# Performance work log

Hardware: AMD Instinct MI355X
Metric: run time of the kernel (lower is better)

The kernel has to match this reference:

```python
import jax, jax.numpy as jnp
import numpy as np

B, D_IN, H, V_TOT, T = 131072, 128, 256, 6, 6  # total_vocab = vocab_size+1 = 6


def setup_inputs() -> dict:
    key = jax.random.key(0)
    ks = jax.random.split(key, 16)
    s = 0.02
    return {
        "x": jax.random.normal(ks[0], (B, D_IN), jnp.float32),
        "W_enc": jax.random.normal(ks[1], (D_IN, H), jnp.float32) * s,
        "b_enc": jnp.zeros((H,), jnp.float32),
        "W_embed": jax.random.normal(ks[2], (V_TOT, H), jnp.float32) * s,
        "b_embed": jnp.zeros((H,), jnp.float32),
        "W_z": jax.random.normal(ks[3], (2 * H, H), jnp.float32) * s,
        "b_z": jnp.zeros((H,), jnp.float32),
        "W_r": jax.random.normal(ks[4], (2 * H, H), jnp.float32) * s,
        "b_r": jnp.zeros((H,), jnp.float32),
        "W_h": jax.random.normal(ks[5], (2 * H, H), jnp.float32) * s,
        "b_h": jnp.zeros((H,), jnp.float32),
        "W_out": jax.random.normal(ks[6], (H, V_TOT), jnp.float32) * s,
        "b_out": jnp.zeros((V_TOT,), jnp.float32),
        "start_embed": jax.random.normal(ks[7], (H,), jnp.float32) * 0.01,
    }


def reference(x, W_enc, b_enc, W_embed, b_embed, W_z, b_z, W_r, b_r, W_h, b_h,
              W_out, b_out, start_embed):
    h0 = x @ W_enc + b_enc                      # encoder: (B, H)
    bsz = h0.shape[0]
    keys = jax.random.split(jax.random.key(42), T)

    def gru(xin, h):
        c = jnp.concatenate([xin, h], axis=-1)
        z = jax.nn.sigmoid(c @ W_z + b_z)
        r = jax.nn.sigmoid(c @ W_r + b_r)
        cr = jnp.concatenate([xin, r * h], axis=-1)
        h_t = jnp.tanh(cr @ W_h + b_h)
        return (1 - z) * h + z * h_t

    def step(carry, key_t):
        h, prev_embed, total_lp, stopped, lengths = carry
        h = gru(prev_embed, h)
        logits = h @ W_out + b_out              # (B, V_TOT)
        token = jax.random.categorical(key_t, logits)  # training=True sampling
        logp = jax.nn.log_softmax(logits)
        active = (~stopped).astype(logits.dtype)
        lp = jnp.take_along_axis(logp, token[:, None], axis=1)[:, 0] * active
        total_lp = total_lp + lp
        onehot = jax.nn.one_hot(token, V_TOT, dtype=logits.dtype) * active[:, None]
        is_stop = token == (V_TOT - 1)
        lengths = lengths + ((~stopped) & (~is_stop)).astype(jnp.int32)
        stopped = stopped | is_stop
        prev_embed = jax.lax.stop_gradient(onehot) @ W_embed + b_embed
        return (h, prev_embed, total_lp, stopped, lengths), onehot

    init = (h0,
            jnp.broadcast_to(start_embed, (bsz, H)),
            jnp.zeros((bsz,), h0.dtype),
            jnp.zeros((bsz,), bool),
            jnp.zeros((bsz,), jnp.int32))
    (h, _, total_log_prob, _, lengths), onehots = jax.lax.scan(step, init, keys)
    # onehots: (T, B, V_TOT) -> message (B, T*V_TOT)
    message = jnp.transpose(onehots, (1, 0, 2)).reshape(bsz, T * V_TOT)
    return message, total_log_prob, lengths
```

## Files before the change

kernel.cpp:

```cpp
#include <hip/hip_runtime.h>
#include <stdint.h>

#define NB   131072
#define DIN  128
#define HD   256
#define VT   6
#define TS   6
#define BM   32
#define NTH  256

typedef __attribute__((ext_vector_type(8))) short bfrag;
typedef __attribute__((ext_vector_type(4))) short bh4;
typedef __attribute__((ext_vector_type(4))) float f32x4;

struct Keys { uint32_t a[6]; uint32_t b[6]; };

#define HPS(p, kc, nt, ln2, j) ((((p) * 8 + (kc)) * 1040) + (nt) * 512 + (ln2) * 8 + (j))

__host__ __device__ inline void tf2x32(uint32_t k0, uint32_t k1,
                                       uint32_t c0, uint32_t c1,
                                       uint32_t& o0, uint32_t& o1) {
  uint32_t ks2 = k0 ^ k1 ^ 0x1BD11BDAu;
  uint32_t x0 = c0 + k0, x1 = c1 + k1;
#define TFR(d) { x0 += x1; x1 = (x1 << (d)) | (x1 >> (32 - (d))); x1 ^= x0; }
  TFR(13) TFR(15) TFR(26) TFR(6)
  x0 += k1;  x1 += ks2 + 1u;
  TFR(17) TFR(29) TFR(16) TFR(24)
  x0 += ks2; x1 += k0 + 2u;
  TFR(13) TFR(15) TFR(26) TFR(6)
  x0 += k0;  x1 += k1 + 3u;
  TFR(17) TFR(29) TFR(16) TFR(24)
  x0 += k1;  x1 += ks2 + 4u;
  TFR(13) TFR(15) TFR(26) TFR(6)
  x0 += ks2; x1 += k0 + 5u;
#undef TFR
  o0 = x0; o1 = x1;
}

__device__ __forceinline__ unsigned short f2bf(float x) {
  uint32_t b = __float_as_uint(x);
  uint32_t r = b + 0x7FFFu + ((b >> 16) & 1u);
  return (unsigned short)(r >> 16);
}
__device__ __forceinline__ float bf2f(unsigned short u) {
  return __uint_as_float(((uint32_t)u) << 16);
}
__device__ __forceinline__ float sigf(float v) { return 1.0f / (1.0f + expf(-v)); }

#define MFMA16(a, b, c) __builtin_amdgcn_mfma_f32_16x16x32_bf16((a), (b), (c), 0, 0, 0)

__device__ __forceinline__ f32x4 prod6(const bfrag A[3], bfrag B0, bfrag B1, bfrag B2,
                                       f32x4 c) {
  c = MFMA16(A[0], B0, c);
  c = MFMA16(A[0], B1, c);
  c = MFMA16(A[1], B0, c);
  c = MFMA16(A[1], B1, c);
  c = MFMA16(A[0], B2, c);
  c = MFMA16(A[2], B0, c);
  return c;
}

__global__ void pre_kernel(const float* __restrict__ W_enc,
                           const float* __restrict__ W_embed,
                           const float* __restrict__ b_embed,
                           const float* __restrict__ start_embed,
                           const float* __restrict__ W_z, const float* __restrict__ b_z,
                           const float* __restrict__ W_r, const float* __restrict__ b_r,
                           const float* __restrict__ W_h, const float* __restrict__ b_h,
                           float* __restrict__ pre,
                           unsigned short* __restrict__ encf,
                           unsigned short* __restrict__ zf,
                           unsigned short* __restrict__ rf,
                           unsigned short* __restrict__ hf) {
  const int bid = blockIdx.x;
  if (bid < 24) {
    __shared__ float xin[HD];
    const int c = bid & 7, g = bid >> 3, j = threadIdx.x;
    float v;
    if (c < 6)       v = W_embed[c * HD + j] + b_embed[j];
    else if (c == 6) v = b_embed[j];
    else             v = start_embed[j];
    xin[j] = v;
    __syncthreads();
    const float* Wg = (g == 0) ? W_z : (g == 1) ? W_r : W_h;
    const float* bg = (g == 0) ? b_z : (g == 1) ? b_r : b_h;
    float acc = bg[j];
    for (int k = 0; k < HD; ++k) acc += xin[k] * Wg[k * HD + j];
    pre[(g * 8 + c) * HD + j] = acc;
    return;
  }
  int id = (bid - 24) * 256 + threadIdx.x;
  const float* src; unsigned short* dst; int kc, mt, lane, KC, krow0;
  if (id < 4096) {
    lane = id & 63; mt = (id >> 6) & 15; kc = id >> 10;
    src = W_enc; dst = encf; KC = 4; krow0 = 0;
  } else {
    int rem = id - 4096; int g = rem >> 13; int rr = rem & 8191;
    lane = rr & 63; mt = (rr >> 6) & 15; kc = rr >> 10;
    src = (g == 0) ? W_z : (g == 1) ? W_r : W_h;
    dst = (g == 0) ? zf  : (g == 1) ? rf  : hf;
    KC = 8; krow0 = 256;
  }
  const int m  = mt * 16 + (lane & 15);
  const int k0 = kc * 32 + ((lane >> 4) & 3) * 8;
  __align__(16) unsigned short P[3][8];
#pragma unroll
  for (int j = 0; j < 8; ++j) {
    float w = src[(size_t)(krow0 + k0 + j) * HD + m];
    unsigned short h1 = f2bf(w);  float r1 = w - bf2f(h1);
    unsigned short h2 = f2bf(r1); float r2 = r1 - bf2f(h2);
    P[0][j] = h1; P[1][j] = h2; P[2][j] = f2bf(r2);
  }
  for (int p = 0; p < 3; ++p) {
    unsigned short* d = dst + ((size_t)(p * KC + kc) * 16 + mt) * 512 + (size_t)lane * 8;
    *(uint4*)d = *(const uint4*)P[p];
  }
}

template<int KC, int NG>
__device__ __forceinline__ void gemm_pass(const unsigned short* __restrict__ f0,
                                          const unsigned short* __restrict__ f1,
                                          const unsigned short* hp_s,
                                          int wave, int lane,
                                          f32x4 acc0[4][2], f32x4 acc1[4][2]) {
#pragma unroll 1
  for (int kc = 0; kc < KC; ++kc) {
    bfrag B[3][2];
#pragma unroll
    for (int p = 0; p < 3; ++p)
#pragma unroll
      for (int nt = 0; nt < 2; ++nt)
        B[p][nt] = *(const bfrag*)&hp_s[HPS(p, kc, nt, lane, 0)];
#pragma unroll
    for (int mtl = 0; mtl < 4; ++mtl) {
      const int fo = (kc * 16 + wave * 4 + mtl) * 512 + lane * 8;
      bfrag A0[3], A1[3];
#pragma unroll
      for (int p = 0; p < 3; ++p) A0[p] = *(const bfrag*)(f0 + fo + p * (KC * 8192));
      if (NG == 2) {
#pragma unroll
        for (int p = 0; p < 3; ++p) A1[p] = *(const bfrag*)(f1 + fo + p * (KC * 8192));
      }
#pragma unroll
      for (int nt = 0; nt < 2; ++nt) {
        acc0[mtl][nt] = prod6(A0, B[0][nt], B[1][nt], B[2][nt], acc0[mtl][nt]);
        if (NG == 2)
          acc1[mtl][nt] = prod6(A1, B[0][nt], B[1][nt], B[2][nt], acc1[mtl][nt]);
      }
    }
  }
}

__launch_bounds__(NTH, 2)
__global__ void main_kernel(const float* __restrict__ x,
                            const float* __restrict__ b_enc,
                            const float* __restrict__ W_out,
                            const float* __restrict__ b_out,
                            const float* __restrict__ pre,
                            const unsigned short* __restrict__ encf,
                            const unsigned short* __restrict__ zf,
                            const unsigned short* __restrict__ rf,
                            const unsigned short* __restrict__ hf,
                            float* __restrict__ out, Keys keys) {
  __shared__ __align__(16) unsigned short hp_s[3 * 8 * 1040];
  __shared__ __align__(16) float wout2[VT * 8 * 40];
  __shared__ unsigned state[BM];
  __shared__ float tlp[BM];

  const int tid = threadIdx.x;
  const int wave = tid >> 6, lane = tid & 63;
  const int ln = lane & 15, qk = lane >> 4;
  const int b0 = blockIdx.x * BM;

  for (int i = tid; i < VT * HD; i += NTH) {
    int k = i & 255, v = i >> 8;
    wout2[(v * 8 + (k >> 5)) * 40 + (k & 31)] = W_out[k * VT + v];
  }
  if (tid < BM) { state[tid] = 7u; tlp[tid] = 0.f; }

  for (int i = tid; i < BM * DIN; i += NTH) {
    int row = i >> 7, k = i & 127;
    float v = x[(size_t)(b0 + row) * DIN + k];
    unsigned short h1 = f2bf(v);  float r1 = v - bf2f(h1);
    unsigned short h2 = f2bf(r1); float r2 = r1 - bf2f(h2);
    int kc = k >> 5, nt = row >> 4, lp = (row & 15) + 16 * ((k >> 3) & 3), j = k & 7;
    hp_s[HPS(0, kc, nt, lp, j)] = h1;
    hp_s[HPS(1, kc, nt, lp, j)] = h2;
    hp_s[HPS(2, kc, nt, lp, j)] = f2bf(r2);
  }
  __syncthreads();

  f32x4 acc0[4][2], acc1[4][2], z_s[4][2], hold[4][2];

#pragma unroll
  for (int mtl = 0; mtl < 4; ++mtl) {
    int mb = wave * 64 + mtl * 16 + qk * 4;
    f32x4 be = *(const f32x4*)&b_enc[mb];
#pragma unroll
    for (int nt = 0; nt < 2; ++nt) acc0[mtl][nt] = be;
  }
  gemm_pass<4, 1>(encf, nullptr, hp_s, wave, lane, acc0, acc1);
  __syncthreads();
#pragma unroll
  for (int mtl = 0; mtl < 4; ++mtl) {
    int mb = wave * 64 + mtl * 16 + qk * 4;
    int kc = mb >> 5, hi2 = (mb >> 3) & 3, j0 = mb & 7;
#pragma unroll
    for (int nt = 0; nt < 2; ++nt) {
      int lp = ln + 16 * hi2;
      bh4 P0, P1, P2;
#pragma unroll
      for (int j = 0; j < 4; ++j) {
        float v = acc0[mtl][nt][j];
        unsigned short h1 = f2bf(v);  float r1 = v - bf2f(h1);
        unsigned short h2 = f2bf(r1); float r2 = r1 - bf2f(h2);
        P0[j] = (short)h1; P1[j] = (short)h2; P2[j] = (short)f2bf(r2);
      }
      *(bh4*)&hp_s[HPS(0, kc, nt, lp, j0)] = P0;
      *(bh4*)&hp_s[HPS(1, kc, nt, lp, j0)] = P1;
      *(bh4*)&hp_s[HPS(2, kc, nt, lp, j0)] = P2;
    }
  }
  __syncthreads();

#pragma unroll 1
  for (int t = 0; t < TS; ++t) {
#pragma unroll
    for (int mtl = 0; mtl < 4; ++mtl) {
      int mb = wave * 64 + mtl * 16 + qk * 4;
#pragma unroll
      for (int nt = 0; nt < 2; ++nt) {
        int code = (int)(state[nt * 16 + ln] & 7u);
        acc0[mtl][nt] = *(const f32x4*)&pre[(0 * 8 + code) * 256 + mb];
        acc1[mtl][nt] = *(const f32x4*)&pre[(1 * 8 + code) * 256 + mb];
      }
    }
    gemm_pass<8, 2>(zf, rf, hp_s, wave, lane, acc0, acc1);
    __syncthreads();
#pragma unroll
    for (int mtl = 0; mtl < 4; ++mtl) {
      int mb = wave * 64 + mtl * 16 + qk * 4;
      int kc = mb >> 5, hi2 = (mb >> 3) & 3, j0 = mb & 7;
#pragma unroll
      for (int nt = 0; nt < 2; ++nt) {
        int lp = ln + 16 * hi2;
        bh4 H0 = *(const bh4*)&hp_s[HPS(0, kc, nt, lp, j0)];
        bh4 H1 = *(const bh4*)&hp_s[HPS(1, kc, nt, lp, j0)];
        bh4 H2 = *(const bh4*)&hp_s[HPS(2, kc, nt, lp, j0)];
        f32x4 ho, zv;
        bh4 P0, P1, P2;
#pragma unroll
        for (int j = 0; j < 4; ++j) {
          float hv = bf2f((unsigned short)H0[j]) + bf2f((unsigned short)H1[j])
                   + bf2f((unsigned short)H2[j]);
          ho[j] = hv;
          zv[j] = sigf(acc0[mtl][nt][j]);
          float rhv = sigf(acc1[mtl][nt][j]) * hv;
          unsigned short h1 = f2bf(rhv); float r1 = rhv - bf2f(h1);
          unsigned short h2 = f2bf(r1);  float r2 = r1 - bf2f(h2);
          P0[j] = (short)h1; P1[j] = (short)h2; P2[j] = (short)f2bf(r2);
        }
        z_s[mtl][nt] = zv; hold[mtl][nt] = ho;
        *(bh4*)&hp_s[HPS(0, kc, nt, lp, j0)] = P0;
        *(bh4*)&hp_s[HPS(1, kc, nt, lp, j0)] = P1;
        *(bh4*)&hp_s[HPS(2, kc, nt, lp, j0)] = P2;
      }
    }
    __syncthreads();

#pragma unroll
    for (int mtl = 0; mtl < 4; ++mtl) {
      int mb = wave * 64 + mtl * 16 + qk * 4;
#pragma unroll
      for (int nt = 0; nt < 2; ++nt) {
        int code = (int)(state[nt * 16 + ln] & 7u);
        acc0[mtl][nt] = *(const f32x4*)&pre[(2 * 8 + code) * 256 + mb];
      }
    }
    gemm_pass<8, 1>(hf, nullptr, hp_s, wave, lane, acc0, acc1);
    __syncthreads();
#pragma unroll
    for (int mtl = 0; mtl < 4; ++mtl) {
      int mb = wave * 64 + mtl * 16 + qk * 4;
      int kc = mb >> 5, hi2 = (mb >> 3) & 3, j0 = mb & 7;
#pragma unroll
      for (int nt = 0; nt < 2; ++nt) {
        int lp = ln + 16 * hi2;
        f32x4 z = z_s[mtl][nt], ho = hold[mtl][nt];
        bh4 P0, P1, P2;
#pragma unroll
        for (int j = 0; j < 4; ++j) {
          float ht = tanhf(acc0[mtl][nt][j]);
          float hn = (1.0f - z[j]) * ho[j] + z[j] * ht;
          unsigned short h1 = f2bf(hn); float r1 = hn - bf2f(h1);
          unsigned short h2 = f2bf(r1); float r2 = r1 - bf2f(h2);
          P0[j] = (short)h1; P1[j] = (short)h2; P2[j] = (short)f2bf(r2);
        }
        *(bh4*)&hp_s[HPS(0, kc, nt, lp, j0)] = P0;
        *(bh4*)&hp_s[HPS(1, kc, nt, lp, j0)] = P1;
        *(bh4*)&hp_s[HPS(2, kc, nt, lp, j0)] = P2;
      }
    }
    __syncthreads();

    {
      const int m = tid >> 3, q = tid & 7;
      float l[VT] = {0.f, 0.f, 0.f, 0.f, 0.f, 0.f};
#pragma unroll
      for (int c8 = 0; c8 < 4; ++c8) {
        bfrag H0 = *(const bfrag*)&hp_s[HPS(0, q, m >> 4, (m & 15) + 16 * c8, 0)];
        bfrag H1 = *(const bfrag*)&hp_s[HPS(1, q, m >> 4, (m & 15) + 16 * c8, 0)];
        bfrag H2 = *(const bfrag*)&hp_s[HPS(2, q, m >> 4, (m & 15) + 16 * c8, 0)];
        float hv[8];
#pragma unroll
        for (int j = 0; j < 8; ++j)
          hv[j] = bf2f((unsigned short)H0[j]) + bf2f((unsigned short)H1[j])
                + bf2f((unsigned short)H2[j]);
#pragma unroll
        for (int v = 0; v < VT; ++v) {
          f32x4 w0 = *(const f32x4*)&wout2[(v * 8 + q) * 40 + c8 * 8];
          f32x4 w1 = *(const f32x4*)&wout2[(v * 8 + q) * 40 + c8 * 8 + 4];
          l[v] += hv[0] * w0[0] + hv[1] * w0[1] + hv[2] * w0[2] + hv[3] * w0[3]
                + hv[4] * w1[0] + hv[5] * w1[1] + hv[6] * w1[2] + hv[7] * w1[3];
        }
      }
#pragma unroll
      for (int v = 0; v < VT; ++v) {
        l[v] += __shfl_xor(l[v], 1, 64);
        l[v] += __shfl_xor(l[v], 2, 64);
        l[v] += __shfl_xor(l[v], 4, 64);
      }
      if (q == 0) {
        const int row = b0 + m;
        unsigned st = state[m];
        if (!(st & 8u)) {
#pragma unroll
          for (int v = 0; v < VT; ++v) l[v] += b_out[v];
          const uint32_t k0 = keys.a[t], k1 = keys.b[t];
          float best = 0.f; int tok = 0;
#pragma unroll
          for (int v = 0; v < VT; ++v) {
            uint32_t j = (uint32_t)row * 6u + (uint32_t)v;
            uint32_t o0, o1;
            tf2x32(k0, k1, 0u, j, o0, o1);
            uint32_t bits = o0 ^ o1;
            float f = __uint_as_float((bits >> 9) | 0x3f800000u) - 1.0f;
            float u = (f > 0.f) ? f : 1.175494350822288e-38f;
            float lg1 = (float)log((double)u);
            float lg2 = (float)log((double)(-lg1));
            float val = l[v] + (-lg2);
            if (v == 0 || val > best) { best = val; tok = v; }
          }
          float lmax = l[0];
#pragma unroll
          for (int v = 1; v < VT; ++v) lmax = fmaxf(lmax, l[v]);
          float s = 0.f;
#pragma unroll
          for (int v = 0; v < VT; ++v) s += expf(l[v] - lmax);
          float lp = (l[tok] - lmax) - logf(s);
          tlp[m] += lp;
          const bool is_stop = (tok == VT - 1);
          unsigned len = ((st >> 4) & 7u) + (is_stop ? 0u : 1u);
#pragma unroll
          for (int v = 0; v < VT; ++v)
            out[(size_t)row * (TS * VT) + t * VT + v] = (v == tok) ? 1.0f : 0.0f;
          state[m] = (unsigned)tok | (is_stop ? 8u : 0u) | (len << 4);
        } else {
#pragma unroll
          for (int v = 0; v < VT; ++v)
            out[(size_t)row * (TS * VT) + t * VT + v] = 0.0f;
          state[m] = 6u | 8u | (st & 0x70u);
        }
      }
    }
    __syncthreads();
  }

  if (tid < BM) {
    const int row = b0 + tid;
    out[(size_t)NB * (TS * VT) + row]      = tlp[tid];
    out[(size_t)NB * (TS * VT) + NB + row] = (float)((state[tid] >> 4) & 7u);
  }
}

extern "C" void kernel_launch(void* const* d_in, const int* in_sizes, int n_in,
                              void* d_out, int out_size, void* d_ws, size_t ws_size,
                              hipStream_t stream) {
  (void)in_sizes; (void)n_in; (void)out_size; (void)ws_size;
  const float* x          = (const float*)d_in[0];
  const float* W_enc      = (const float*)d_in[1];
  const float* b_enc      = (const float*)d_in[2];
  const float* W_embed    = (const float*)d_in[3];
  const float* b_embed    = (const float*)d_in[4];
  const float* W_z        = (const float*)d_in[5];
  const float* b_z        = (const float*)d_in[6];
  const float* W_r        = (const float*)d_in[7];
  const float* b_r        = (const float*)d_in[8];
  const float* W_h        = (const float*)d_in[9];
  const float* b_h        = (const float*)d_in[10];
  const float* W_out      = (const float*)d_in[11];
  const float* b_out      = (const float*)d_in[12];
  const float* start_embed= (const float*)d_in[13];
  float* out = (float*)d_out;

  float* pre = (float*)d_ws;
  unsigned short* encf = (unsigned short*)((char*)d_ws + 24576);
  unsigned short* zfb  = (unsigned short*)((char*)d_ws + 221184);
  unsigned short* rfb  = (unsigned short*)((char*)d_ws + 614400);
  unsigned short* hfb  = (unsigned short*)((char*)d_ws + 1007616);

  pre_kernel<<<136, 256, 0, stream>>>(W_enc, W_embed, b_embed, start_embed,
                                      W_z, b_z, W_r, b_r, W_h, b_h,
                                      pre, encf, zfb, rfb, hfb);

  Keys K;
  for (int t = 0; t < 6; ++t) {
    uint32_t o0, o1;
    tf2x32(0u, 42u, 0u, (uint32_t)t, o0, o1);
    K.a[t] = o0; K.b[t] = o1;
  }

  main_kernel<<<NB / BM, NTH, 0, stream>>>(x, b_enc, W_out, b_out,
                                           pre, encf, zfb, rfb, hfb, out, K);
}
```

Before: 2.088 ms.

## Double batch tile to 64 rows, keep h in registers, parallelize sampling across lanes

```diff
diff --git a/kernel.cpp b/kernel.cpp
--- a/kernel.cpp
+++ b/kernel.cpp
@@ -6,8 +6,8 @@
 #define HD   256
 #define VT   6
 #define TS   6
-#define BM   32
-#define NTH  256
+#define BM   64
+#define NTH  512
 
 typedef __attribute__((ext_vector_type(8))) short bfrag;
 typedef __attribute__((ext_vector_type(4))) short bh4;
@@ -15,7 +15,7 @@
 
 struct Keys { uint32_t a[6]; uint32_t b[6]; };
 
-#define HPS(p, kc, nt, ln2, j) ((((p) * 8 + (kc)) * 1040) + (nt) * 512 + (ln2) * 8 + (j))
+#define HPS(p, kc, nt, lp, j) ((((p) * 8 + (kc)) * 2064) + (nt) * 512 + (lp) * 8 + (j))
 
 __host__ __device__ inline void tf2x32(uint32_t k0, uint32_t k1,
                                        uint32_t c0, uint32_t c1,
@@ -122,18 +122,18 @@
                                           const unsigned short* __restrict__ f1,
                                           const unsigned short* hp_s,
                                           int wave, int lane,
-                                          f32x4 acc0[4][2], f32x4 acc1[4][2]) {
+                                          f32x4 acc0[2][4], f32x4 acc1[2][4]) {
 #pragma unroll 1
   for (int kc = 0; kc < KC; ++kc) {
-    bfrag B[3][2];
+    bfrag B[3][4];
 #pragma unroll
     for (int p = 0; p < 3; ++p)
 #pragma unroll
-      for (int nt = 0; nt < 2; ++nt)
+      for (int nt = 0; nt < 4; ++nt)
         B[p][nt] = *(const bfrag*)&hp_s[HPS(p, kc, nt, lane, 0)];
 #pragma unroll
-    for (int mtl = 0; mtl < 4; ++mtl) {
-      const int fo = (kc * 16 + wave * 4 + mtl) * 512 + lane * 8;
+    for (int mtl = 0; mtl < 2; ++mtl) {
+      const int fo = (kc * 16 + wave * 2 + mtl) * 512 + lane * 8;
       bfrag A0[3], A1[3];
 #pragma unroll
       for (int p = 0; p < 3; ++p) A0[p] = *(const bfrag*)(f0 + fo + p * (KC * 8192));
@@ -142,7 +142,7 @@
         for (int p = 0; p < 3; ++p) A1[p] = *(const bfrag*)(f1 + fo + p * (KC * 8192));
       }
 #pragma unroll
-      for (int nt = 0; nt < 2; ++nt) {
+      for (int nt = 0; nt < 4; ++nt) {
         acc0[mtl][nt] = prod6(A0, B[0][nt], B[1][nt], B[2][nt], acc0[mtl][nt]);
         if (NG == 2)
           acc1[mtl][nt] = prod6(A1, B[0][nt], B[1][nt], B[2][nt], acc1[mtl][nt]);
@@ -162,8 +162,9 @@
                             const unsigned short* __restrict__ rf,
                             const unsigned short* __restrict__ hf,
                             float* __restrict__ out, Keys keys) {
-  __shared__ __align__(16) unsigned short hp_s[3 * 8 * 1040];
+  __shared__ __align__(16) unsigned short hp_s[3 * 8 * 2064];
   __shared__ __align__(16) float wout2[VT * 8 * 40];
+  __shared__ float boutL[8];
   __shared__ unsigned state[BM];
   __shared__ float tlp[BM];
 
@@ -176,6 +177,7 @@
     int k = i & 255, v = i >> 8;
     wout2[(v * 8 + (k >> 5)) * 40 + (k & 31)] = W_out[k * VT + v];
   }
+  if (tid < 8) boutL[tid] = (tid < VT) ? b_out[tid] : 0.f;
   if (tid < BM) { state[tid] = 7u; tlp[tid] = 0.f; }
 
   for (int i = tid; i < BM * DIN; i += NTH) {
@@ -190,28 +192,29 @@
   }
   __syncthreads();
 
-  f32x4 acc0[4][2], acc1[4][2], z_s[4][2], hold[4][2];
-
-#pragma unroll
-  for (int mtl = 0; mtl < 4; ++mtl) {
-    int mb = wave * 64 + mtl * 16 + qk * 4;
+  f32x4 acc0[2][4], acc1[2][4], z_s[2][4], hold[2][4];
+
+#pragma unroll
+  for (int mtl = 0; mtl < 2; ++mtl) {
+    int mb = (wave * 2 + mtl) * 16 + qk * 4;
     f32x4 be = *(const f32x4*)&b_enc[mb];
 #pragma unroll
-    for (int nt = 0; nt < 2; ++nt) acc0[mtl][nt] = be;
+    for (int nt = 0; nt < 4; ++nt) acc0[mtl][nt] = be;
   }
   gemm_pass<4, 1>(encf, nullptr, hp_s, wave, lane, acc0, acc1);
   __syncthreads();
 #pragma unroll
-  for (int mtl = 0; mtl < 4; ++mtl) {
-    int mb = wave * 64 + mtl * 16 + qk * 4;
-    int kc = mb >> 5, hi2 = (mb >> 3) & 3, j0 = mb & 7;
-#pragma unroll
-    for (int nt = 0; nt < 2; ++nt) {
-      int lp = ln + 16 * hi2;
+  for (int mtl = 0; mtl < 2; ++mtl) {
+    int mb = (wave * 2 + mtl) * 16 + qk * 4;
+    int kc = mb >> 5, hi2 = (mb >> 3) & 3, j0 = mb & 7, lp = ln + 16 * hi2;
+#pragma unroll
+    for (int nt = 0; nt < 4; ++nt) {
+      f32x4 o = acc0[mtl][nt];
+      hold[mtl][nt] = o;
       bh4 P0, P1, P2;
 #pragma unroll
       for (int j = 0; j < 4; ++j) {
-        float v = acc0[mtl][nt][j];
+        float v = o[j];
         unsigned short h1 = f2bf(v);  float r1 = v - bf2f(h1);
         unsigned short h2 = f2bf(r1); float r2 = r1 - bf2f(h2);
         P0[j] = (short)h1; P1[j] = (short)h2; P2[j] = (short)f2bf(r2);
@@ -226,10 +229,10 @@
 #pragma unroll 1
   for (int t = 0; t < TS; ++t) {
 #pragma unroll
-    for (int mtl = 0; mtl < 4; ++mtl) {
-      int mb = wave * 64 + mtl * 16 + qk * 4;
-#pragma unroll
-      for (int nt = 0; nt < 2; ++nt) {
+    for (int mtl = 0; mtl < 2; ++mtl) {
+      int mb = (wave * 2 + mtl) * 16 + qk * 4;
+#pragma unroll
+      for (int nt = 0; nt < 4; ++nt) {
         int code = (int)(state[nt * 16 + ln] & 7u);
         acc0[mtl][nt] = *(const f32x4*)&pre[(0 * 8 + code) * 256 + mb];
         acc1[mtl][nt] = *(const f32x4*)&pre[(1 * 8 + code) * 256 + mb];
@@ -238,29 +241,23 @@
     gemm_pass<8, 2>(zf, rf, hp_s, wave, lane, acc0, acc1);
     __syncthreads();
 #pragma unroll
-    for (int mtl = 0; mtl < 4; ++mtl) {
-      int mb = wave * 64 + mtl * 16 + qk * 4;
-      int kc = mb >> 5, hi2 = (mb >> 3) & 3, j0 = mb & 7;
-#pragma unroll
-      for (int nt = 0; nt < 2; ++nt) {
-        int lp = ln + 16 * hi2;
-        bh4 H0 = *(const bh4*)&hp_s[HPS(0, kc, nt, lp, j0)];
-        bh4 H1 = *(const bh4*)&hp_s[HPS(1, kc, nt, lp, j0)];
-        bh4 H2 = *(const bh4*)&hp_s[HPS(2, kc, nt, lp, j0)];
-        f32x4 ho, zv;
+    for (int mtl = 0; mtl < 2; ++mtl) {
+      int mb = (wave * 2 + mtl) * 16 + qk * 4;
+      int kc = mb >> 5, hi2 = (mb >> 3) & 3, j0 = mb & 7, lp = ln + 16 * hi2;
+#pragma unroll
+      for (int nt = 0; nt < 4; ++nt) {
+        f32x4 ho = hold[mtl][nt];
+        f32x4 zv;
         bh4 P0, P1, P2;
 #pragma unroll
         for (int j = 0; j < 4; ++j) {
-          float hv = bf2f((unsigned short)H0[j]) + bf2f((unsigned short)H1[j])
-                   + bf2f((unsigned short)H2[j]);
-          ho[j] = hv;
           zv[j] = sigf(acc0[mtl][nt][j]);
-          float rhv = sigf(acc1[mtl][nt][j]) * hv;
+          float rhv = sigf(acc1[mtl][nt][j]) * ho[j];
           unsigned short h1 = f2bf(rhv); float r1 = rhv - bf2f(h1);
           unsigned short h2 = f2bf(r1);  float r2 = r1 - bf2f(h2);
           P0[j] = (short)h1; P1[j] = (short)h2; P2[j] = (short)f2bf(r2);
         }
-        z_s[mtl][nt] = zv; hold[mtl][nt] = ho;
+        z_s[mtl][nt] = zv;
         *(bh4*)&hp_s[HPS(0, kc, nt, lp, j0)] = P0;
         *(bh4*)&hp_s[HPS(1, kc, nt, lp, j0)] = P1;
         *(bh4*)&hp_s[HPS(2, kc, nt, lp, j0)] = P2;
@@ -269,10 +266,10 @@
     __syncthreads();
 
 #pragma unroll
-    for (int mtl = 0; mtl < 4; ++mtl) {
-      int mb = wave * 64 + mtl * 16 + qk * 4;
-#pragma unroll
-      for (int nt = 0; nt < 2; ++nt) {
+    for (int mtl = 0; mtl < 2; ++mtl) {
+      int mb = (wave * 2 + mtl) * 16 + qk * 4;
+#pragma unroll
+      for (int nt = 0; nt < 4; ++nt) {
         int code = (int)(state[nt * 16 + ln] & 7u);
         acc0[mtl][nt] = *(const f32x4*)&pre[(2 * 8 + code) * 256 + mb];
       }
@@ -280,22 +277,22 @@
     gemm_pass<8, 1>(hf, nullptr, hp_s, wave, lane, acc0, acc1);
     __syncthreads();
 #pragma unroll
-    for (int mtl = 0; mtl < 4; ++mtl) {
-      int mb = wave * 64 + mtl * 16 + qk * 4;
-      int kc = mb >> 5, hi2 = (mb >> 3) & 3, j0 = mb & 7;
-#pragma unroll
-      for (int nt = 0; nt < 2; ++nt) {
-        int lp = ln + 16 * hi2;
-        f32x4 z = z_s[mtl][nt], ho = hold[mtl][nt];
+    for (int mtl = 0; mtl < 2; ++mtl) {
+      int mb = (wave * 2 + mtl) * 16 + qk * 4;
+      int kc = mb >> 5, hi2 = (mb >> 3) & 3, j0 = mb & 7, lp = ln + 16 * hi2;
+#pragma unroll
+      for (int nt = 0; nt < 4; ++nt) {
+        f32x4 z = z_s[mtl][nt], ho = hold[mtl][nt], hn;
         bh4 P0, P1, P2;
 #pragma unroll
         for (int j = 0; j < 4; ++j) {
           float ht = tanhf(acc0[mtl][nt][j]);
-          float hn = (1.0f - z[j]) * ho[j] + z[j] * ht;
-          unsigned short h1 = f2bf(hn); float r1 = hn - bf2f(h1);
-          unsigned short h2 = f2bf(r1); float r2 = r1 - bf2f(h2);
+          hn[j] = (1.0f - z[j]) * ho[j] + z[j] * ht;
+          unsigned short h1 = f2bf(hn[j]); float r1 = hn[j] - bf2f(h1);
+          unsigned short h2 = f2bf(r1);    float r2 = r1 - bf2f(h2);
           P0[j] = (short)h1; P1[j] = (short)h2; P2[j] = (short)f2bf(r2);
         }
+        hold[mtl][nt] = hn;
         *(bh4*)&hp_s[HPS(0, kc, nt, lp, j0)] = P0;
         *(bh4*)&hp_s[HPS(1, kc, nt, lp, j0)] = P1;
         *(bh4*)&hp_s[HPS(2, kc, nt, lp, j0)] = P2;
@@ -330,27 +327,33 @@
         l[v] += __shfl_xor(l[v], 2, 64);
         l[v] += __shfl_xor(l[v], 4, 64);
       }
+      const int row = b0 + m;
+      const int vq = (q < VT) ? q : 0;
+      float lq = l[vq] + boutL[vq];
+      {
+        uint32_t j = (uint32_t)row * 6u + (uint32_t)vq;
+        uint32_t o0, o1;
+        tf2x32(keys.a[t], keys.b[t], 0u, j, o0, o1);
+        uint32_t bits = o0 ^ o1;
+        float f = __uint_as_float((bits >> 9) | 0x3f800000u) - 1.0f;
+        float u = (f > 0.f) ? f : 1.175494350822288e-38f;
+        float lg1 = (float)log((double)u);
+        float lg2 = (float)log((double)(-lg1));
+        lq = lq + (-lg2);
+      }
+      float vv[VT];
+      const int lbase = lane & ~7;
+#pragma unroll
+      for (int v = 0; v < VT; ++v) vv[v] = __shfl(lq, lbase + v, 64);
       if (q == 0) {
-        const int row = b0 + m;
         unsigned st = state[m];
         if (!(st & 8u)) {
 #pragma unroll
-          for (int v = 0; v < VT; ++v) l[v] += b_out[v];
-          const uint32_t k0 = keys.a[t], k1 = keys.b[t];
+          for (int v = 0; v < VT; ++v) l[v] += boutL[v];
           float best = 0.f; int tok = 0;
 #pragma unroll
-          for (int v = 0; v < VT; ++v) {
-            uint32_t j = (uint32_t)row * 6u + (uint32_t)v;
-            uint32_t o0, o1;
-            tf2x32(k0, k1, 0u, j, o0, o1);
-            uint32_t bits = o0 ^ o1;
-            float f = __uint_as_float((bits >> 9) | 0x3f800000u) - 1.0f;
-            float u = (f > 0.f) ? f : 1.175494350822288e-38f;
-            float lg1 = (float)log((double)u);
-            float lg2 = (float)log((double)(-lg1));
-            float val = l[v] + (-lg2);
-            if (v == 0 || val > best) { best = val; tok = v; }
-          }
+          for (int v = 0; v < VT; ++v)
+            if (v == 0 || vv[v] > best) { best = vv[v]; tok = v; }
           float lmax = l[0];
 #pragma unroll
           for (int v = 1; v < VT; ++v) lmax = fmaxf(lmax, l[v]);
```

Result: faster. 2.033 ms (-2.6%).

## Compute output logits with MFMA, overlap Gumbel noise generation, keep h in registers

Applied to the files above, without the earlier changes.

```diff
diff --git a/kernel.cpp b/kernel.cpp
--- a/kernel.cpp
+++ b/kernel.cpp
@@ -15,7 +15,7 @@
 
 struct Keys { uint32_t a[6]; uint32_t b[6]; };
 
-#define HPS(p, kc, nt, ln2, j) ((((p) * 8 + (kc)) * 1040) + (nt) * 512 + (ln2) * 8 + (j))
+#define HPS(p, kc, nt, lp, j) ((((p) * 8 + (kc)) * 1040) + (nt) * 512 + (lp) * 8 + (j))
 
 __host__ __device__ inline void tf2x32(uint32_t k0, uint32_t k1,
                                        uint32_t c0, uint32_t c1,
@@ -67,11 +67,13 @@
                            const float* __restrict__ W_z, const float* __restrict__ b_z,
                            const float* __restrict__ W_r, const float* __restrict__ b_r,
                            const float* __restrict__ W_h, const float* __restrict__ b_h,
+                           const float* __restrict__ W_out,
                            float* __restrict__ pre,
                            unsigned short* __restrict__ encf,
                            unsigned short* __restrict__ zf,
                            unsigned short* __restrict__ rf,
-                           unsigned short* __restrict__ hf) {
+                           unsigned short* __restrict__ hf,
+                           unsigned short* __restrict__ woutf) {
   const int bid = blockIdx.x;
   if (bid < 24) {
     __shared__ float xin[HD];
@@ -87,6 +89,24 @@
     float acc = bg[j];
     for (int k = 0; k < HD; ++k) acc += xin[k] * Wg[k * HD + j];
     pre[(g * 8 + c) * HD + j] = acc;
+    return;
+  }
+  if (bid >= 136) {
+    int id2 = (bid - 136) * 256 + threadIdx.x;
+    int kc = id2 >> 6, lane = id2 & 63;
+    int m = lane & 15, k0 = kc * 32 + ((lane >> 4) & 3) * 8;
+    __align__(16) unsigned short P[3][8];
+#pragma unroll
+    for (int j = 0; j < 8; ++j) {
+      float w = (m < VT) ? W_out[(size_t)(k0 + j) * VT + m] : 0.f;
+      unsigned short h1 = f2bf(w);  float r1 = w - bf2f(h1);
+      unsigned short h2 = f2bf(r1); float r2 = r1 - bf2f(h2);
+      P[0][j] = h1; P[1][j] = h2; P[2][j] = f2bf(r2);
+    }
+    for (int p = 0; p < 3; ++p) {
+      unsigned short* d = woutf + ((size_t)(p * 8 + kc) * 512) + (size_t)lane * 8;
+      *(uint4*)d = *(const uint4*)P[p];
+    }
     return;
   }
   int id = (bid - 24) * 256 + threadIdx.x;
@@ -151,19 +171,40 @@
   }
 }
 
+__device__ __forceinline__ void gen_gumbel(float* __restrict__ gmb, int s, int b0,
+                                           int tile, int lane,
+                                           uint32_t ka, uint32_t kb) {
+  uint32_t basej = (uint32_t)(b0 + tile * 16) * 6u;
+#pragma unroll
+  for (int rep = 0; rep < 2; ++rep) {
+    int d = rep * 64 + lane;
+    if (d < 96) {
+      uint32_t o0, o1;
+      tf2x32(ka, kb, 0u, basej + (uint32_t)d, o0, o1);
+      uint32_t bits = o0 ^ o1;
+      float f = __uint_as_float((bits >> 9) | 0x3f800000u) - 1.0f;
+      float u = (f > 0.f) ? f : 1.175494350822288e-38f;
+      float lg1 = (float)log((double)u);
+      float lg2 = (float)log((double)(-lg1));
+      gmb[((s & 1) * 32 + tile * 16 + d / 6) * 6 + (d % 6)] = -lg2;
+    }
+  }
+}
+
 __launch_bounds__(NTH, 2)
 __global__ void main_kernel(const float* __restrict__ x,
                             const float* __restrict__ b_enc,
-                            const float* __restrict__ W_out,
                             const float* __restrict__ b_out,
                             const float* __restrict__ pre,
                             const unsigned short* __restrict__ encf,
                             const unsigned short* __restrict__ zf,
                             const unsigned short* __restrict__ rf,
                             const unsigned short* __restrict__ hf,
+                            const unsigned short* __restrict__ woutf,
                             float* __restrict__ out, Keys keys) {
   __shared__ __align__(16) unsigned short hp_s[3 * 8 * 1040];
-  __shared__ __align__(16) float wout2[VT * 8 * 40];
+  __shared__ float gmb_s[2 * 32 * 6];
+  __shared__ float boutL[16];
   __shared__ unsigned state[BM];
   __shared__ float tlp[BM];
 
@@ -172,10 +213,7 @@
   const int ln = lane & 15, qk = lane >> 4;
   const int b0 = blockIdx.x * BM;
 
-  for (int i = tid; i < VT * HD; i += NTH) {
-    int k = i & 255, v = i >> 8;
-    wout2[(v * 8 + (k >> 5)) * 40 + (k & 31)] = W_out[k * VT + v];
-  }
+  if (tid < 16) boutL[tid] = (tid < VT) ? b_out[tid] : 0.f;
   if (tid < BM) { state[tid] = 7u; tlp[tid] = 0.f; }
 
   for (int i = tid; i < BM * DIN; i += NTH) {
@@ -188,13 +226,14 @@
     hp_s[HPS(1, kc, nt, lp, j)] = h2;
     hp_s[HPS(2, kc, nt, lp, j)] = f2bf(r2);
   }
+  if (wave >= 2) gen_gumbel(gmb_s, 0, b0, wave - 2, lane, keys.a[0], keys.b[0]);
   __syncthreads();
 
   f32x4 acc0[4][2], acc1[4][2], z_s[4][2], hold[4][2];
 
 #pragma unroll
   for (int mtl = 0; mtl < 4; ++mtl) {
-    int mb = wave * 64 + mtl * 16 + qk * 4;
+    int mb = (wave * 4 + mtl) * 16 + qk * 4;
     f32x4 be = *(const f32x4*)&b_enc[mb];
 #pragma unroll
     for (int nt = 0; nt < 2; ++nt) acc0[mtl][nt] = be;
@@ -203,15 +242,16 @@
   __syncthreads();
 #pragma unroll
   for (int mtl = 0; mtl < 4; ++mtl) {
-    int mb = wave * 64 + mtl * 16 + qk * 4;
-    int kc = mb >> 5, hi2 = (mb >> 3) & 3, j0 = mb & 7;
+    int mb = (wave * 4 + mtl) * 16 + qk * 4;
+    int kc = mb >> 5, hi2 = (mb >> 3) & 3, j0 = mb & 7, lp = ln + 16 * hi2;
 #pragma unroll
     for (int nt = 0; nt < 2; ++nt) {
-      int lp = ln + 16 * hi2;
+      f32x4 o = acc0[mtl][nt];
+      hold[mtl][nt] = o;
       bh4 P0, P1, P2;
 #pragma unroll
       for (int j = 0; j < 4; ++j) {
-        float v = acc0[mtl][nt][j];
+        float v = o[j];
         unsigned short h1 = f2bf(v);  float r1 = v - bf2f(h1);
         unsigned short h2 = f2bf(r1); float r2 = r1 - bf2f(h2);
         P0[j] = (short)h1; P1[j] = (short)h2; P2[j] = (short)f2bf(r2);
@@ -227,7 +267,7 @@
   for (int t = 0; t < TS; ++t) {
 #pragma unroll
     for (int mtl = 0; mtl < 4; ++mtl) {
-      int mb = wave * 64 + mtl * 16 + qk * 4;
+      int mb = (wave * 4 + mtl) * 16 + qk * 4;
 #pragma unroll
       for (int nt = 0; nt < 2; ++nt) {
         int code = (int)(state[nt * 16 + ln] & 7u);
@@ -239,28 +279,22 @@
     __syncthreads();
 #pragma unroll
     for (int mtl = 0; mtl < 4; ++mtl) {
-      int mb = wave * 64 + mtl * 16 + qk * 4;
-      int kc = mb >> 5, hi2 = (mb >> 3) & 3, j0 = mb & 7;
+      int mb = (wave * 4 + mtl) * 16 + qk * 4;
+      int kc = mb >> 5, hi2 = (mb >> 3) & 3, j0 = mb & 7, lp = ln + 16 * hi2;
 #pragma unroll
       for (int nt = 0; nt < 2; ++nt) {
-        int lp = ln + 16 * hi2;
-        bh4 H0 = *(const bh4*)&hp_s[HPS(0, kc, nt, lp, j0)];
-        bh4 H1 = *(const bh4*)&hp_s[HPS(1, kc, nt, lp, j0)];
-        bh4 H2 = *(const bh4*)&hp_s[HPS(2, kc, nt, lp, j0)];
-        f32x4 ho, zv;
+        f32x4 ho = hold[mtl][nt];
+        f32x4 zv;
         bh4 P0, P1, P2;
 #pragma unroll
         for (int j = 0; j < 4; ++j) {
-          float hv = bf2f((unsigned short)H0[j]) + bf2f((unsigned short)H1[j])
-                   + bf2f((unsigned short)H2[j]);
-          ho[j] = hv;
           zv[j] = sigf(acc0[mtl][nt][j]);
-          float rhv = sigf(acc1[mtl][nt][j]) * hv;
+          float rhv = sigf(acc1[mtl][nt][j]) * ho[j];
           unsigned short h1 = f2bf(rhv); float r1 = rhv - bf2f(h1);
           unsigned short h2 = f2bf(r1);  float r2 = r1 - bf2f(h2);
           P0[j] = (short)h1; P1[j] = (short)h2; P2[j] = (short)f2bf(r2);
         }
-        z_s[mtl][nt] = zv; hold[mtl][nt] = ho;
+        z_s[mtl][nt] = zv;
         *(bh4*)&hp_s[HPS(0, kc, nt, lp, j0)] = P0;
         *(bh4*)&hp_s[HPS(1, kc, nt, lp, j0)] = P1;
         *(bh4*)&hp_s[HPS(2, kc, nt, lp, j0)] = P2;
@@ -270,7 +304,7 @@
 
 #pragma unroll
     for (int mtl = 0; mtl < 4; ++mtl) {
-      int mb = wave * 64 + mtl * 16 + qk * 4;
+      int mb = (wave * 4 + mtl) * 16 + qk * 4;
 #pragma unroll
       for (int nt = 0; nt < 2; ++nt) {
         int code = (int)(state[nt * 16 + ln] & 7u);
@@ -281,21 +315,21 @@
     __syncthreads();
 #pragma unroll
     for (int mtl = 0; mtl < 4; ++mtl) {
-      int mb = wave * 64 + mtl * 16 + qk * 4;
-      int kc = mb >> 5, hi2 = (mb >> 3) & 3, j0 = mb & 7;
+      int mb = (wave * 4 + mtl) * 16 + qk * 4;
+      int kc = mb >> 5, hi2 = (mb >> 3) & 3, j0 = mb & 7, lp = ln + 16 * hi2;
 #pragma unroll
       for (int nt = 0; nt < 2; ++nt) {
-        int lp = ln + 16 * hi2;
-        f32x4 z = z_s[mtl][nt], ho = hold[mtl][nt];
+        f32x4 z = z_s[mtl][nt], ho = hold[mtl][nt], hn;
         bh4 P0, P1, P2;
 #pragma unroll
         for (int j = 0; j < 4; ++j) {
           float ht = tanhf(acc0[mtl][nt][j]);
-          float hn = (1.0f - z[j]) * ho[j] + z[j] * ht;
-          unsigned short h1 = f2bf(hn); float r1 = hn - bf2f(h1);
-          unsigned short h2 = f2bf(r1); float r2 = r1 - bf2f(h2);
+          hn[j] = (1.0f - z[j]) * ho[j] + z[j] * ht;
+          unsigned short h1 = f2bf(hn[j]); float r1 = hn[j] - bf2f(h1);
+          unsigned short h2 = f2bf(r1);    float r2 = r1 - bf2f(h2);
           P0[j] = (short)h1; P1[j] = (short)h2; P2[j] = (short)f2bf(r2);
         }
+        hold[mtl][nt] = hn;
         *(bh4*)&hp_s[HPS(0, kc, nt, lp, j0)] = P0;
         *(bh4*)&hp_s[HPS(1, kc, nt, lp, j0)] = P1;
         *(bh4*)&hp_s[HPS(2, kc, nt, lp, j0)] = P2;
@@ -303,52 +337,33 @@
     }
     __syncthreads();
 
-    {
-      const int m = tid >> 3, q = tid & 7;
-      float l[VT] = {0.f, 0.f, 0.f, 0.f, 0.f, 0.f};
-#pragma unroll
-      for (int c8 = 0; c8 < 4; ++c8) {
-        bfrag H0 = *(const bfrag*)&hp_s[HPS(0, q, m >> 4, (m & 15) + 16 * c8, 0)];
-        bfrag H1 = *(const bfrag*)&hp_s[HPS(1, q, m >> 4, (m & 15) + 16 * c8, 0)];
-        bfrag H2 = *(const bfrag*)&hp_s[HPS(2, q, m >> 4, (m & 15) + 16 * c8, 0)];
-        float hv[8];
-#pragma unroll
-        for (int j = 0; j < 8; ++j)
-          hv[j] = bf2f((unsigned short)H0[j]) + bf2f((unsigned short)H1[j])
-                + bf2f((unsigned short)H2[j]);
-#pragma unroll
-        for (int v = 0; v < VT; ++v) {
-          f32x4 w0 = *(const f32x4*)&wout2[(v * 8 + q) * 40 + c8 * 8];
-          f32x4 w1 = *(const f32x4*)&wout2[(v * 8 + q) * 40 + c8 * 8 + 4];
-          l[v] += hv[0] * w0[0] + hv[1] * w0[1] + hv[2] * w0[2] + hv[3] * w0[3]
-                + hv[4] * w1[0] + hv[5] * w1[1] + hv[6] * w1[2] + hv[7] * w1[3];
-        }
-      }
-#pragma unroll
-      for (int v = 0; v < VT; ++v) {
-        l[v] += __shfl_xor(l[v], 1, 64);
-        l[v] += __shfl_xor(l[v], 2, 64);
-        l[v] += __shfl_xor(l[v], 4, 64);
-      }
-      if (q == 0) {
+    if (wave < 2) {
+      f32x4 lacc;
+#pragma unroll
+      for (int j = 0; j < 4; ++j) lacc[j] = boutL[qk * 4 + j];
+#pragma unroll 1
+      for (int kc = 0; kc < 8; ++kc) {
+        bfrag B0 = *(const bfrag*)&hp_s[HPS(0, kc, wave, lane, 0)];
+        bfrag B1 = *(const bfrag*)&hp_s[HPS(1, kc, wave, lane, 0)];
+        bfrag B2 = *(const bfrag*)&hp_s[HPS(2, kc, wave, lane, 0)];
+        bfrag A[3];
+#pragma unroll
+        for (int p = 0; p < 3; ++p)
+          A[p] = *(const bfrag*)(woutf + (p * 8 + kc) * 512 + lane * 8);
+        lacc = prod6(A, B0, B1, B2, lacc);
+      }
+      float l4 = __shfl(lacc[0], ln + 16, 64);
+      float l5 = __shfl(lacc[1], ln + 16, 64);
+      if (qk == 0) {
+        const int m = wave * 16 + ln;
         const int row = b0 + m;
         unsigned st = state[m];
         if (!(st & 8u)) {
-#pragma unroll
-          for (int v = 0; v < VT; ++v) l[v] += b_out[v];
-          const uint32_t k0 = keys.a[t], k1 = keys.b[t];
+          float l[VT] = {lacc[0], lacc[1], lacc[2], lacc[3], l4, l5};
           float best = 0.f; int tok = 0;
 #pragma unroll
           for (int v = 0; v < VT; ++v) {
-            uint32_t j = (uint32_t)row * 6u + (uint32_t)v;
-            uint32_t o0, o1;
-            tf2x32(k0, k1, 0u, j, o0, o1);
-            uint32_t bits = o0 ^ o1;
-            float f = __uint_as_float((bits >> 9) | 0x3f800000u) - 1.0f;
-            float u = (f > 0.f) ? f : 1.175494350822288e-38f;
-            float lg1 = (float)log((double)u);
-            float lg2 = (float)log((double)(-lg1));
-            float val = l[v] + (-lg2);
+            float val = l[v] + gmb_s[((t & 1) * 32 + m) * 6 + v];
             if (v == 0 || val > best) { best = val; tok = v; }
           }
           float lmax = l[0];
@@ -372,6 +387,8 @@
           state[m] = 6u | 8u | (st & 0x70u);
         }
       }
+    } else if (t + 1 < TS) {
+      gen_gumbel(gmb_s, t + 1, b0, wave - 2, lane, keys.a[t + 1], keys.b[t + 1]);
     }
     __syncthreads();
   }
@@ -408,10 +425,11 @@
   unsigned short* zfb  = (unsigned short*)((char*)d_ws + 221184);
   unsigned short* rfb  = (unsigned short*)((char*)d_ws + 614400);
   unsigned short* hfb  = (unsigned short*)((char*)d_ws + 1007616);
-
-  pre_kernel<<<136, 256, 0, stream>>>(W_enc, W_embed, b_embed, start_embed,
-                                      W_z, b_z, W_r, b_r, W_h, b_h,
-                                      pre, encf, zfb, rfb, hfb);
+  unsigned short* wof  = (unsigned short*)((char*)d_ws + 1400832);
+
+  pre_kernel<<<138, 256, 0, stream>>>(W_enc, W_embed, b_embed, start_embed,
+                                      W_z, b_z, W_r, b_r, W_h, b_h, W_out,
+                                      pre, encf, zfb, rfb, hfb, wof);
 
   Keys K;
   for (int t = 0; t < 6; ++t) {
@@ -420,6 +438,6 @@
     K.a[t] = o0; K.b[t] = o1;
   }
 
-  main_kernel<<<NB / BM, NTH, 0, stream>>>(x, b_enc, W_out, b_out,
-                                           pre, encf, zfb, rfb, hfb, out, K);
-}
+  main_kernel<<<NB / BM, NTH, 0, stream>>>(x, b_enc, b_out,
+                                           pre, encf, zfb, rfb, hfb, wof, out, K);
+}
```

Measured after the change: 1.916 ms. 8.2% less time.
